# Optimization experiments

Hardware: AMD Instinct MI355X
Metric: run time of the kernel (lower is better)

The kernel has to match this reference:

```python
import jax, jax.numpy as jnp
import numpy as np

N = 100_000      # nodes
E = 800_000      # edges (avg degree 8)
D_IN = 16        # embedding_dimension
H = 128          # hidden_dimension
OUT = 3          # out_dim
NEG_SLOPE = 0.01 # LeakyReLU default


def setup_inputs() -> dict:
    key = jax.random.key(0)
    ks = jax.random.split(key, 9)
    s = 0.05
    return {
        "feature": jax.random.normal(ks[0], (N, D_IN), jnp.float32),
        "edge_index": jax.random.randint(ks[1], (2, E), 0, N, dtype=jnp.int64),
        "edge_type": jax.random.randint(ks[2], (E,), 0, 2, dtype=jnp.int64),
        "W_in": jax.random.normal(ks[3], (D_IN, H), jnp.float32) * s,
        "b_in": jnp.zeros((H,), jnp.float32),
        "W1": jax.random.normal(ks[4], (H, H), jnp.float32) * s,
        "b1": jnp.zeros((H,), jnp.float32),
        "W2": jax.random.normal(ks[5], (H, H), jnp.float32) * s,
        "b2": jnp.zeros((H,), jnp.float32),
        "W_out": jax.random.normal(ks[6], (H, OUT), jnp.float32) * s,
        "b_out": jnp.zeros((OUT,), jnp.float32),
    }


def gcn_conv(x, W, b, src, dst, n):
    """PyG GCNConv: linear -> add self-loops -> D^-1/2 A D^-1/2 aggregation -> bias."""
    h = x @ W                                   # [N, H]
    loop = jnp.arange(n, dtype=src.dtype)
    src_sl = jnp.concatenate([src, loop])       # [E+N]
    dst_sl = jnp.concatenate([dst, loop])
    deg = jax.ops.segment_sum(jnp.ones_like(dst_sl, dtype=h.dtype), dst_sl, num_segments=n)
    dinv = jax.lax.rsqrt(jnp.maximum(deg, 1.0))  # deg >= 1 due to self-loops
    norm = dinv[src_sl] * dinv[dst_sl]          # [E+N]
    msg = h[src_sl] * norm[:, None]             # gather + scale, [E+N, H]
    out = jax.ops.segment_sum(msg, dst_sl, num_segments=n)  # scatter-add
    return out + b


def reference(feature, edge_index, edge_type, W_in, b_in, W1, b1, W2, b2, W_out, b_out):
    # edge_type is accepted but unused, exactly as in the torch forward.
    x = jax.nn.leaky_relu(feature.astype(jnp.float32) @ W_in + b_in, NEG_SLOPE)
    src, dst = edge_index[0], edge_index[1]
    x = gcn_conv(x, W1, b1, src, dst, N)
    # F.dropout with training=False is identity (inference path)
    x = gcn_conv(x, W2, b2, src, dst, N)
    return x @ W_out + b_out
```

## Files before the change

kernel.cpp:

```cpp
#include <hip/hip_runtime.h>
#include <hip/hip_bf16.h>
#include <cstdint>

#define DIN 16
#define HD  128
#define RNG 2048
#define LB  11
#define MAXB 64
#define PB  256

static __device__ __forceinline__ void fma4(float4& a, float s, const float4 v) {
    a.x = fmaf(s, v.x, a.x);
    a.y = fmaf(s, v.y, a.y);
    a.z = fmaf(s, v.z, a.z);
    a.w = fmaf(s, v.w, a.w);
}
static __device__ __forceinline__ void add4(float4& a, const float4 v) {
    a.x += v.x; a.y += v.y; a.z += v.z; a.w += v.w;
}
static __device__ __forceinline__ void lrelu4(float4& h) {
    h.x = h.x > 0.f ? h.x : 0.01f * h.x;
    h.y = h.y > 0.f ? h.y : 0.01f * h.y;
    h.z = h.z > 0.f ? h.z : 0.01f * h.z;
    h.w = h.w > 0.f ? h.w : 0.01f * h.w;
}

__global__ __launch_bounds__(256) void k_histfold(const int* __restrict__ dst,
                                                  int* __restrict__ hist,
                                                  int E, int R, int CHK,
                                                  const float* __restrict__ W1,
                                                  const float* __restrict__ b1,
                                                  const float* __restrict__ W2,
                                                  const float* __restrict__ b2,
                                                  const float* __restrict__ Wout,
                                                  const float* __restrict__ bout,
                                                  float* __restrict__ Wcp,
                                                  float* __restrict__ cbuf) {
    int tid = threadIdx.x;
    if (blockIdx.x < PB) {
        __shared__ int h[MAXB];
        for (int i = tid; i < R; i += 256) h[i] = 0;
        __syncthreads();
        int e0 = blockIdx.x * CHK;
        int e1 = e0 + CHK; if (e1 > E) e1 = E;
        for (int e = e0 + tid; e < e1; e += 256) atomicAdd(&h[dst[e] >> LB], 1);
        __syncthreads();
        for (int i = tid; i < R; i += 256) hist[i * PB + blockIdx.x] = h[i];
        return;
    }
    __shared__ float sT[HD * 3];
    for (int idx = tid; idx < HD * 3; idx += 256) {
        int k = idx / 3, o = idx - 3 * k;
        float s = 0.f;
        for (int j = 0; j < HD; j++) s = fmaf(W2[k * HD + j], Wout[j * 3 + o], s);
        sT[idx] = s;
    }
    if (tid < 3) {
        float s = bout[tid];
        for (int j = 0; j < HD; j++) s = fmaf(b2[j], Wout[j * 3 + tid], s);
        cbuf[3 + tid] = s;
    }
    __syncthreads();
    if (tid < 3) {
        float s = 0.f;
        for (int j = 0; j < HD; j++) s = fmaf(b1[j], sT[j * 3 + tid], s);
        cbuf[tid] = s;
    }
    for (int idx = tid; idx < HD * 3; idx += 256) {
        int k = idx / 3, o = idx - 3 * k;
        float s = 0.f;
        for (int j = 0; j < HD; j++) s = fmaf(W1[k * HD + j], sT[j * 3 + o], s);
        Wcp[k * 4 + o] = s;
    }
    for (int idx = tid; idx < HD; idx += 256) Wcp[idx * 4 + 3] = 0.f;
}

__global__ __launch_bounds__(1024) void k_scanmlp(int* __restrict__ hist, int nh,
                                                  const float* __restrict__ F,
                                                  const float* __restrict__ Win,
                                                  const float* __restrict__ bin,
                                                  const float4* __restrict__ Wcp,
                                                  float4* __restrict__ Y, int N) {
    int tid = threadIdx.x;
    if (blockIdx.x == 0) {
        __shared__ int sd[1024];
        int CH = (nh + 1023) / 1024;
        int c0 = tid * CH;
        int c1 = c0 + CH; if (c1 > nh) c1 = nh;
        int sum = 0;
        for (int i = c0; i < c1; i++) sum += hist[i];
        sd[tid] = sum;
        __syncthreads();
        for (int off = 1; off < 1024; off <<= 1) {
            int t = (tid >= off) ? sd[tid - off] : 0;
            __syncthreads();
            sd[tid] += t;
            __syncthreads();
        }
        int base = sd[tid] - sum;
        for (int i = c0; i < c1; i++) { int t = hist[i]; hist[i] = base; base += t; }
        return;
    }
    __shared__ float4 sWinT[DIN * HD / 4];
    __shared__ float4 sWcT[HD];
    __shared__ float4 sBin[HD / 4];
    __shared__ float  sF[128 * DIN];
    if (tid < DIN * HD / 4) {
        int k = tid >> 5, rem = tid & 31, l = rem >> 1, c = rem & 1;
        sWinT[k * 32 + c * 16 + l] = ((const float4*)Win)[tid];
    } else if (tid < DIN * HD / 4 + HD) {
        int i = tid - DIN * HD / 4;
        sWcT[(i & 7) * 16 + (i >> 3)] = Wcp[i];
    } else if (tid < DIN * HD / 4 + HD + HD / 4) {
        int i = tid - DIN * HD / 4 - HD;
        sBin[i] = ((const float4*)bin)[i];
    }
    int base = (blockIdx.x - 1) * 128;
    {
        int n0 = base + (tid >> 4);
        sF[tid] = (n0 < N) ? F[(size_t)base * DIN + tid] : 0.f;
        int n1 = base + ((tid + 1024) >> 4);
        sF[tid + 1024] = (n1 < N) ? F[(size_t)base * DIN + tid + 1024] : 0.f;
    }
    __syncthreads();
    int l = tid & 15;
    int g = tid >> 4;
    int nodeA = base + 2 * g;
    int nodeB = nodeA + 1;
    if (nodeA >= N) return;
    float4 a0 = sBin[l * 2 + 0], a1 = sBin[l * 2 + 1];
    float4 b0 = a0, b1 = a1;
    #pragma unroll
    for (int k = 0; k < DIN; k++) {
        float4 w0 = sWinT[k * 32 + l];
        float4 w1 = sWinT[k * 32 + 16 + l];
        float fA = sF[(2 * g) * DIN + k];
        float fB = sF[(2 * g + 1) * DIN + k];
        fma4(a0, fA, w0); fma4(a1, fA, w1);
        fma4(b0, fB, w0); fma4(b1, fB, w1);
    }
    lrelu4(a0); lrelu4(a1); lrelu4(b0); lrelu4(b1);
    float hA[8] = {a0.x, a0.y, a0.z, a0.w, a1.x, a1.y, a1.z, a1.w};
    float hB[8] = {b0.x, b0.y, b0.z, b0.w, b1.x, b1.y, b1.z, b1.w};
    float pA0 = 0.f, pA1 = 0.f, pA2 = 0.f, pB0 = 0.f, pB1 = 0.f, pB2 = 0.f;
    #pragma unroll
    for (int jj = 0; jj < 8; jj++) {
        float4 wc = sWcT[jj * 16 + l];
        pA0 = fmaf(hA[jj], wc.x, pA0);
        pA1 = fmaf(hA[jj], wc.y, pA1);
        pA2 = fmaf(hA[jj], wc.z, pA2);
        pB0 = fmaf(hB[jj], wc.x, pB0);
        pB1 = fmaf(hB[jj], wc.y, pB1);
        pB2 = fmaf(hB[jj], wc.z, pB2);
    }
    #pragma unroll
    for (int off = 8; off > 0; off >>= 1) {
        pA0 += __shfl_down(pA0, off, 16);
        pA1 += __shfl_down(pA1, off, 16);
        pA2 += __shfl_down(pA2, off, 16);
        pB0 += __shfl_down(pB0, off, 16);
        pB1 += __shfl_down(pB1, off, 16);
        pB2 += __shfl_down(pB2, off, 16);
    }
    if (l == 0) {
        Y[nodeA] = make_float4(pA0, pA1, pA2, 1.0f);
        if (nodeB < N) Y[nodeB] = make_float4(pB0, pB1, pB2, 1.0f);
    }
}

__global__ __launch_bounds__(256) void k_part(const int* __restrict__ src,
                                              const int* __restrict__ dst,
                                              const int* __restrict__ off,
                                              int* __restrict__ ebin,
                                              int E, int R, int CHK) {
    __shared__ int cur[MAXB];
    int tid = threadIdx.x;
    int b = blockIdx.x;
    for (int i = tid; i < R; i += 256) cur[i] = off[i * PB + b];
    __syncthreads();
    int e0 = b * CHK;
    int e1 = e0 + CHK; if (e1 > E) e1 = E;
    for (int e = e0 + tid; e < e1; e += 256) {
        int s = src[e], d = dst[e];
        int pos = atomicAdd(&cur[d >> LB], 1);
        ebin[pos] = (s << LB) | (d & (RNG - 1));
    }
}

__global__ __launch_bounds__(1024) void k_csr(const int* __restrict__ ebin,
                                              const int* __restrict__ off,
                                              const float4* __restrict__ Y,
                                              int* __restrict__ rowptr,
                                              int* __restrict__ ecsr,
                                              float* __restrict__ dinv,
                                              float4* __restrict__ Ys,
                                              int N, int E, int R) {
    __shared__ int c[RNG];
    __shared__ int swv[16];
    int tid = threadIdx.x;
    int b = blockIdx.x;
    c[tid] = 0; c[tid + 1024] = 0;
    __syncthreads();
    int e0 = off[b * PB];
    int e1 = (b + 1 < R) ? off[(b + 1) * PB] : E;
    for (int e = e0 + tid; e < e1; e += 1024) atomicAdd(&c[ebin[e] & (RNG - 1)], 1);
    __syncthreads();
    int v0 = c[2 * tid], v1 = c[2 * tid + 1];
    int ts = v0 + v1;
    int lane = tid & 63, wid = tid >> 6;
    int sc = ts;
    #pragma unroll
    for (int o = 1; o < 64; o <<= 1) {
        int t = __shfl_up(sc, o, 64);
        if (lane >= o) sc += t;
    }
    if (lane == 63) swv[wid] = sc;
    __syncthreads();
    if (tid < 16) {
        int v = swv[tid];
        int s2 = v;
        #pragma unroll
        for (int o = 1; o < 16; o <<= 1) {
            int t = __shfl_up(s2, o, 16);
            if (tid >= o) s2 += t;
        }
        swv[tid] = s2 - v;
    }
    __syncthreads();
    int excl = sc - ts + swv[wid];
    int rp0 = e0 + excl;
    int rp1 = rp0 + v0;
    int n0 = b * RNG + 2 * tid;
    if (n0 <= N) rowptr[n0] = rp0;
    if (n0 + 1 <= N) rowptr[n0 + 1] = rp1;
    if (b == R - 1 && tid == 1023) rowptr[N] = E;
    if (n0 < N) {
        float di = rsqrtf((float)v0 + 1.0f);
        dinv[n0] = di;
        float4 y = Y[n0];
        Ys[n0] = make_float4(di * y.x, di * y.y, di * y.z, di);
    }
    if (n0 + 1 < N) {
        float di = rsqrtf((float)v1 + 1.0f);
        dinv[n0 + 1] = di;
        float4 y = Y[n0 + 1];
        Ys[n0 + 1] = make_float4(di * y.x, di * y.y, di * y.z, di);
    }
    c[2 * tid] = rp0;
    c[2 * tid + 1] = rp1;
    __syncthreads();
    for (int e = e0 + tid; e < e1; e += 1024) {
        int ed = ebin[e];
        int pos = atomicAdd(&c[ed & (RNG - 1)], 1);
        ecsr[pos] = ed >> LB;
    }
    if (b == 0 && tid < 16) ecsr[E + tid] = 0;
}

__global__ __launch_bounds__(256) void k_aggA(const int* __restrict__ rowptr,
                                              const int* __restrict__ ecsr,
                                              const float4* __restrict__ Ys,
                                              const float* __restrict__ dinv,
                                              float4* __restrict__ Z1s, int N) {
    int n = blockIdx.x * blockDim.x + threadIdx.x;
    if (n >= N) return;
    int beg = rowptr[n], end = rowptr[n + 1];
    int deg = end - beg;
    float4 acc = Ys[n];
    int4 q0 = *(const int4*)(ecsr + beg);
    int4 q1 = *(const int4*)(ecsr + beg + 4);
    int4 q2 = *(const int4*)(ecsr + beg + 8);
    int si[12] = {q0.x, q0.y, q0.z, q0.w, q1.x, q1.y, q1.z, q1.w,
                  q2.x, q2.y, q2.z, q2.w};
    float4 g[12];
    #pragma unroll
    for (int k = 0; k < 12; k++) g[k] = Ys[si[k]];
    #pragma unroll
    for (int k = 0; k < 12; k++) if (k < deg) add4(acc, g[k]);
    for (int j = beg + 12; j < end; j++) add4(acc, Ys[ecsr[j]]);
    float di = dinv[n];
    float d2 = di * di;
    Z1s[n] = make_float4(d2 * acc.x, d2 * acc.y, d2 * acc.z, d2 * acc.w);
}

__global__ __launch_bounds__(256) void k_aggB(const int* __restrict__ rowptr,
                                              const int* __restrict__ ecsr,
                                              const float4* __restrict__ Z1s,
                                              const float* __restrict__ dinv,
                                              const float* __restrict__ cbuf,
                                              float* __restrict__ out, int N) {
    int n = blockIdx.x * blockDim.x + threadIdx.x;
    if (n >= N) return;
    int beg = rowptr[n], end = rowptr[n + 1];
    int deg = end - beg;
    float4 acc = Z1s[n];
    float di = dinv[n];
    float r = acc.w / di;
    int4 q0 = *(const int4*)(ecsr + beg);
    int4 q1 = *(const int4*)(ecsr + beg + 4);
    int4 q2 = *(const int4*)(ecsr + beg + 8);
    int si[12] = {q0.x, q0.y, q0.z, q0.w, q1.x, q1.y, q1.z, q1.w,
                  q2.x, q2.y, q2.z, q2.w};
    float4 g[12];
    #pragma unroll
    for (int k = 0; k < 12; k++) g[k] = Z1s[si[k]];
    #pragma unroll
    for (int k = 0; k < 12; k++) if (k < deg) add4(acc, g[k]);
    for (int j = beg + 12; j < end; j++) add4(acc, Z1s[ecsr[j]]);
    out[(size_t)n * 3 + 0] = di * acc.x + r * cbuf[0] + cbuf[3];
    out[(size_t)n * 3 + 1] = di * acc.y + r * cbuf[1] + cbuf[4];
    out[(size_t)n * 3 + 2] = di * acc.z + r * cbuf[2] + cbuf[5];
}

extern "C" void kernel_launch(void* const* d_in, const int* in_sizes, int n_in,
                              void* d_out, int out_size, void* d_ws, size_t ws_size,
                              hipStream_t stream) {
    const float* feat = (const float*)d_in[0];
    const int*   ei   = (const int*)d_in[1];
    const float* Win  = (const float*)d_in[3];
    const float* bin  = (const float*)d_in[4];
    const float* W1   = (const float*)d_in[5];
    const float* b1   = (const float*)d_in[6];
    const float* W2   = (const float*)d_in[7];
    const float* b2   = (const float*)d_in[8];
    const float* Wout = (const float*)d_in[9];
    const float* bout = (const float*)d_in[10];
    float* out = (float*)d_out;

    int N = in_sizes[0] / DIN;
    int E = in_sizes[2];
    const int* src = ei;
    const int* dst = ei + E;

    int R = (N + RNG - 1) >> LB;
    int CHK = (E + PB - 1) / PB;
    int NH = R * PB;
    int XB = (N + 127) / 128;

    char* p = (char*)d_ws;
    auto alloc = [&](size_t bytes) -> char* {
        char* q = p;
        p += (bytes + 511) & ~(size_t)511;
        return q;
    };
    int*    hist   = (int*)alloc((size_t)NH * 4);
    int*    ebin   = (int*)alloc((size_t)E * 4);
    int*    ecsr   = (int*)alloc(((size_t)E + 16) * 4);
    int*    rowptr = (int*)alloc((size_t)(N + 1) * 4);
    float4* Y      = (float4*)alloc((size_t)N * 16);
    float4* Ys     = (float4*)alloc((size_t)N * 16);
    float4* Z1s    = (float4*)alloc((size_t)N * 16);
    float*  dinv   = (float*)alloc((size_t)N * 4);
    float*  Wcp    = (float*)alloc(HD * 4 * 4);
    float*  cbuf   = (float*)alloc(8 * 4);

    k_histfold<<<PB + 1, 256, 0, stream>>>(dst, hist, E, R, CHK,
                                           W1, b1, W2, b2, Wout, bout, Wcp, cbuf);
    k_scanmlp<<<1 + XB, 1024, 0, stream>>>(hist, NH, feat, Win, bin,
                                           (const float4*)Wcp, Y, N);
    k_part<<<PB, 256, 0, stream>>>(src, dst, hist, ebin, E, R, CHK);
    k_csr<<<R, 1024, 0, stream>>>(ebin, hist, Y, rowptr, ecsr, dinv, Ys, N, E, R);
    k_aggA<<<(N + 255) / 256, 256, 0, stream>>>(rowptr, ecsr, Ys, dinv, Z1s, N);
    k_aggB<<<(N + 255) / 256, 256, 0, stream>>>(rowptr, ecsr, Z1s, dinv, cbuf, out, N);
}
```

Before: 157.8 us.

## Replace histogram-scan-partition CSR build with atomic bin reservation into fixed-capacity bins

Edge binning by destination range no longer runs a per-block histogram, a global scan and a separate partition pass. Each block now counts its edges per bin, reserves space in a global per-bin counter with atomics, and scatters into fixed-capacity slots of CAP entries per bin. That partition work is fused into the front kernel alongside the input MLP, removing one launch and the scan. The CSR kernel uses smaller bins (512 nodes, 512 threads) and works out each bin's edge offset by reducing the bin counts itself. The cost is extra workspace and an assumption that no bin exceeds CAP edges. That assumption holds only for roughly uniform degree distributions, and edge order within a bin becomes nondeterministic.

```diff
diff --git a/kernel.cpp b/kernel.cpp
--- a/kernel.cpp
+++ b/kernel.cpp
@@ -1,13 +1,13 @@
 #include <hip/hip_runtime.h>
-#include <hip/hip_bf16.h>
 #include <cstdint>
 
 #define DIN 16
 #define HD  128
-#define RNG 2048
-#define LB  11
-#define MAXB 64
-#define PB  256
+#define RNG 512
+#define LB  9
+#define MAXB 256
+#define CAP 8192
+#define PBB 128
 
 static __device__ __forceinline__ void fma4(float4& a, float s, const float4 v) {
     a.x = fmaf(s, v.x, a.x);
@@ -25,29 +25,17 @@
     h.w = h.w > 0.f ? h.w : 0.01f * h.w;
 }
 
-__global__ __launch_bounds__(256) void k_histfold(const int* __restrict__ dst,
-                                                  int* __restrict__ hist,
-                                                  int E, int R, int CHK,
-                                                  const float* __restrict__ W1,
-                                                  const float* __restrict__ b1,
-                                                  const float* __restrict__ W2,
-                                                  const float* __restrict__ b2,
-                                                  const float* __restrict__ Wout,
-                                                  const float* __restrict__ bout,
-                                                  float* __restrict__ Wcp,
-                                                  float* __restrict__ cbuf) {
+__global__ __launch_bounds__(256) void k_init(int* __restrict__ binCnt, int R,
+                                              const float* __restrict__ W1,
+                                              const float* __restrict__ b1,
+                                              const float* __restrict__ W2,
+                                              const float* __restrict__ b2,
+                                              const float* __restrict__ Wout,
+                                              const float* __restrict__ bout,
+                                              float* __restrict__ Wcp,
+                                              float* __restrict__ cbuf) {
     int tid = threadIdx.x;
-    if (blockIdx.x < PB) {
-        __shared__ int h[MAXB];
-        for (int i = tid; i < R; i += 256) h[i] = 0;
-        __syncthreads();
-        int e0 = blockIdx.x * CHK;
-        int e1 = e0 + CHK; if (e1 > E) e1 = E;
-        for (int e = e0 + tid; e < e1; e += 256) atomicAdd(&h[dst[e] >> LB], 1);
-        __syncthreads();
-        for (int i = tid; i < R; i += 256) hist[i * PB + blockIdx.x] = h[i];
-        return;
-    }
+    for (int i = tid; i < R; i += 256) binCnt[i] = 0;
     __shared__ float sT[HD * 3];
     for (int idx = tid; idx < HD * 3; idx += 256) {
         int k = idx / 3, o = idx - 3 * k;
@@ -75,30 +63,39 @@
     for (int idx = tid; idx < HD; idx += 256) Wcp[idx * 4 + 3] = 0.f;
 }
 
-__global__ __launch_bounds__(1024) void k_scanmlp(int* __restrict__ hist, int nh,
-                                                  const float* __restrict__ F,
-                                                  const float* __restrict__ Win,
-                                                  const float* __restrict__ bin,
-                                                  const float4* __restrict__ Wcp,
-                                                  float4* __restrict__ Y, int N) {
+__global__ __launch_bounds__(1024) void k_front(const int* __restrict__ src,
+                                                const int* __restrict__ dst,
+                                                int* __restrict__ binCnt,
+                                                int* __restrict__ ebin,
+                                                int E, int R, int CHK,
+                                                const float* __restrict__ F,
+                                                const float* __restrict__ Win,
+                                                const float* __restrict__ binp,
+                                                const float4* __restrict__ Wcp,
+                                                float4* __restrict__ Y, int N) {
     int tid = threadIdx.x;
-    if (blockIdx.x == 0) {
-        __shared__ int sd[1024];
-        int CH = (nh + 1023) / 1024;
-        int c0 = tid * CH;
-        int c1 = c0 + CH; if (c1 > nh) c1 = nh;
-        int sum = 0;
-        for (int i = c0; i < c1; i++) sum += hist[i];
-        sd[tid] = sum;
+    if (blockIdx.x < PBB) {
+        __shared__ int cnt[MAXB];
+        __shared__ int rsv[MAXB];
+        for (int i = tid; i < R; i += 1024) cnt[i] = 0;
         __syncthreads();
-        for (int off = 1; off < 1024; off <<= 1) {
-            int t = (tid >= off) ? sd[tid - off] : 0;
-            __syncthreads();
-            sd[tid] += t;
-            __syncthreads();
+        int e0 = blockIdx.x * CHK;
+        int e1 = e0 + CHK; if (e1 > E) e1 = E;
+        for (int e = e0 + tid; e < e1; e += 1024) atomicAdd(&cnt[dst[e] >> LB], 1);
+        __syncthreads();
+        for (int i = tid; i < R; i += 1024) {
+            int cc = cnt[i];
+            rsv[i] = cc ? atomicAdd(&binCnt[i], cc) : 0;
         }
-        int base = sd[tid] - sum;
-        for (int i = c0; i < c1; i++) { int t = hist[i]; hist[i] = base; base += t; }
+        __syncthreads();
+        for (int i = tid; i < R; i += 1024) cnt[i] = 0;
+        __syncthreads();
+        for (int e = e0 + tid; e < e1; e += 1024) {
+            int s = src[e], d = dst[e];
+            int bb = d >> LB;
+            int lp = atomicAdd(&cnt[bb], 1);
+            ebin[(size_t)bb * CAP + rsv[bb] + lp] = (s << LB) | (d & (RNG - 1));
+        }
         return;
     }
     __shared__ float4 sWinT[DIN * HD / 4];
@@ -113,9 +110,9 @@
         sWcT[(i & 7) * 16 + (i >> 3)] = Wcp[i];
     } else if (tid < DIN * HD / 4 + HD + HD / 4) {
         int i = tid - DIN * HD / 4 - HD;
-        sBin[i] = ((const float4*)bin)[i];
-    }
-    int base = (blockIdx.x - 1) * 128;
+        sBin[i] = ((const float4*)binp)[i];
+    }
+    int base = (blockIdx.x - PBB) * 128;
     {
         int n0 = base + (tid >> 4);
         sF[tid] = (n0 < N) ? F[(size_t)base * DIN + tid] : 0.f;
@@ -168,47 +165,43 @@
     }
 }
 
-__global__ __launch_bounds__(256) void k_part(const int* __restrict__ src,
-                                              const int* __restrict__ dst,
-                                              const int* __restrict__ off,
-                                              int* __restrict__ ebin,
-                                              int E, int R, int CHK) {
-    __shared__ int cur[MAXB];
+__global__ __launch_bounds__(512) void k_csr(const int* __restrict__ ebin,
+                                             const int* __restrict__ binCnt,
+                                             const float4* __restrict__ Y,
+                                             int* __restrict__ rowptr,
+                                             int* __restrict__ ecsr,
+                                             float* __restrict__ dinv,
+                                             float4* __restrict__ Ys,
+                                             int N, int E, int R) {
+    __shared__ int c[RNG];
+    __shared__ int sb[MAXB];
+    __shared__ int swv[8];
+    __shared__ int se0;
     int tid = threadIdx.x;
     int b = blockIdx.x;
-    for (int i = tid; i < R; i += 256) cur[i] = off[i * PB + b];
-    __syncthreads();
-    int e0 = b * CHK;
-    int e1 = e0 + CHK; if (e1 > E) e1 = E;
-    for (int e = e0 + tid; e < e1; e += 256) {
-        int s = src[e], d = dst[e];
-        int pos = atomicAdd(&cur[d >> LB], 1);
-        ebin[pos] = (s << LB) | (d & (RNG - 1));
-    }
-}
-
-__global__ __launch_bounds__(1024) void k_csr(const int* __restrict__ ebin,
-                                              const int* __restrict__ off,
-                                              const float4* __restrict__ Y,
-                                              int* __restrict__ rowptr,
-                                              int* __restrict__ ecsr,
-                                              float* __restrict__ dinv,
-                                              float4* __restrict__ Ys,
-                                              int N, int E, int R) {
-    __shared__ int c[RNG];
-    __shared__ int swv[16];
-    int tid = threadIdx.x;
-    int b = blockIdx.x;
-    c[tid] = 0; c[tid + 1024] = 0;
-    __syncthreads();
-    int e0 = off[b * PB];
-    int e1 = (b + 1 < R) ? off[(b + 1) * PB] : E;
-    for (int e = e0 + tid; e < e1; e += 1024) atomicAdd(&c[ebin[e] & (RNG - 1)], 1);
-    __syncthreads();
-    int v0 = c[2 * tid], v1 = c[2 * tid + 1];
-    int ts = v0 + v1;
+    c[tid] = 0;
+    if (tid < MAXB) sb[tid] = (tid < R) ? binCnt[tid] : 0;
+    __syncthreads();
+    int cnt = sb[b];
+    int part = (tid < b) ? sb[tid] : 0;
+    #pragma unroll
+    for (int o = 32; o > 0; o >>= 1) part += __shfl_down(part, o, 64);
+    if ((tid & 63) == 0) swv[tid >> 6] = part;
+    __syncthreads();
+    if (tid == 0) {
+        int s = 0;
+        #pragma unroll
+        for (int w = 0; w < 8; w++) s += swv[w];
+        se0 = s;
+    }
+    __syncthreads();
+    int e0 = se0;
+    int ebase = b * CAP;
+    for (int e = tid; e < cnt; e += 512) atomicAdd(&c[ebin[ebase + e] & (RNG - 1)], 1);
+    __syncthreads();
+    int v0 = c[tid];
     int lane = tid & 63, wid = tid >> 6;
-    int sc = ts;
+    int sc = v0;
     #pragma unroll
     for (int o = 1; o < 64; o <<= 1) {
         int t = __shfl_up(sc, o, 64);
@@ -216,41 +209,31 @@
     }
     if (lane == 63) swv[wid] = sc;
     __syncthreads();
-    if (tid < 16) {
+    if (tid < 8) {
         int v = swv[tid];
         int s2 = v;
         #pragma unroll
-        for (int o = 1; o < 16; o <<= 1) {
-            int t = __shfl_up(s2, o, 16);
+        for (int o = 1; o < 8; o <<= 1) {
+            int t = __shfl_up(s2, o, 8);
             if (tid >= o) s2 += t;
         }
         swv[tid] = s2 - v;
     }
     __syncthreads();
-    int excl = sc - ts + swv[wid];
+    int excl = sc - v0 + swv[wid];
     int rp0 = e0 + excl;
-    int rp1 = rp0 + v0;
-    int n0 = b * RNG + 2 * tid;
+    int n0 = b * RNG + tid;
     if (n0 <= N) rowptr[n0] = rp0;
-    if (n0 + 1 <= N) rowptr[n0 + 1] = rp1;
-    if (b == R - 1 && tid == 1023) rowptr[N] = E;
     if (n0 < N) {
         float di = rsqrtf((float)v0 + 1.0f);
         dinv[n0] = di;
         float4 y = Y[n0];
         Ys[n0] = make_float4(di * y.x, di * y.y, di * y.z, di);
     }
-    if (n0 + 1 < N) {
-        float di = rsqrtf((float)v1 + 1.0f);
-        dinv[n0 + 1] = di;
-        float4 y = Y[n0 + 1];
-        Ys[n0 + 1] = make_float4(di * y.x, di * y.y, di * y.z, di);
-    }
-    c[2 * tid] = rp0;
-    c[2 * tid + 1] = rp1;
-    __syncthreads();
-    for (int e = e0 + tid; e < e1; e += 1024) {
-        int ed = ebin[e];
+    c[tid] = rp0;
+    __syncthreads();
+    for (int e = tid; e < cnt; e += 512) {
+        int ed = ebin[ebase + e];
         int pos = atomicAdd(&c[ed & (RNG - 1)], 1);
         ecsr[pos] = ed >> LB;
     }
@@ -318,7 +301,7 @@
     const float* feat = (const float*)d_in[0];
     const int*   ei   = (const int*)d_in[1];
     const float* Win  = (const float*)d_in[3];
-    const float* bin  = (const float*)d_in[4];
+    const float* binp = (const float*)d_in[4];
     const float* W1   = (const float*)d_in[5];
     const float* b1   = (const float*)d_in[6];
     const float* W2   = (const float*)d_in[7];
@@ -333,8 +316,7 @@
     const int* dst = ei + E;
 
     int R = (N + RNG - 1) >> LB;
-    int CHK = (E + PB - 1) / PB;
-    int NH = R * PB;
+    int CHK = (E + PBB - 1) / PBB;
     int XB = (N + 127) / 128;
 
     char* p = (char*)d_ws;
@@ -343,8 +325,8 @@
         p += (bytes + 511) & ~(size_t)511;
         return q;
     };
-    int*    hist   = (int*)alloc((size_t)NH * 4);
-    int*    ebin   = (int*)alloc((size_t)E * 4);
+    int*    binCnt = (int*)alloc((size_t)R * 4);
+    int*    ebin   = (int*)alloc((size_t)R * CAP * 4);
     int*    ecsr   = (int*)alloc(((size_t)E + 16) * 4);
     int*    rowptr = (int*)alloc((size_t)(N + 1) * 4);
     float4* Y      = (float4*)alloc((size_t)N * 16);
@@ -354,12 +336,10 @@
     float*  Wcp    = (float*)alloc(HD * 4 * 4);
     float*  cbuf   = (float*)alloc(8 * 4);
 
-    k_histfold<<<PB + 1, 256, 0, stream>>>(dst, hist, E, R, CHK,
-                                           W1, b1, W2, b2, Wout, bout, Wcp, cbuf);
-    k_scanmlp<<<1 + XB, 1024, 0, stream>>>(hist, NH, feat, Win, bin,
-                                           (const float4*)Wcp, Y, N);
-    k_part<<<PB, 256, 0, stream>>>(src, dst, hist, ebin, E, R, CHK);
-    k_csr<<<R, 1024, 0, stream>>>(ebin, hist, Y, rowptr, ecsr, dinv, Ys, N, E, R);
+    k_init<<<1, 256, 0, stream>>>(binCnt, R, W1, b1, W2, b2, Wout, bout, Wcp, cbuf);
+    k_front<<<PBB + XB, 1024, 0, stream>>>(src, dst, binCnt, ebin, E, R, CHK,
+                                           feat, Win, binp, (const float4*)Wcp, Y, N);
+    k_csr<<<R, 512, 0, stream>>>(ebin, binCnt, Y, rowptr, ecsr, dinv, Ys, N, E, R);
     k_aggA<<<(N + 255) / 256, 256, 0, stream>>>(rowptr, ecsr, Ys, dinv, Z1s, N);
     k_aggB<<<(N + 255) / 256, 256, 0, stream>>>(rowptr, ecsr, Z1s, dinv, cbuf, out, N);
 }
```

After: 145.2 us. 8.0% less time.
